# Kernel tuning notes

Hardware: AMD Instinct MI355X
Metric: run time of the kernel (lower is better)

The kernel has to match this reference:

```python
import jax, jax.numpy as jnp
import numpy as np

EPS = 1e-5


def setup_inputs() -> dict:
    key = jax.random.key(0)
    ks = jax.random.split(key, 7)
    N, M, D, H, DM = 8192, 128, 64, 8, 1024  # tokens, num_memories, d_memory, heads, d_model
    return {
        "query": jax.random.normal(ks[0], (N, DM), dtype=jnp.float32),
        "addresses": jax.random.normal(ks[1], (M, D), dtype=jnp.float32),
        "memories": jax.random.normal(ks[2], (N, M, D), dtype=jnp.float32),
        "Wq": jax.random.normal(ks[3], (DM, H * D), dtype=jnp.float32) / np.sqrt(DM),
        "bq": jax.random.normal(ks[4], (H * D,), dtype=jnp.float32) * 0.01,
        "Wo": jax.random.normal(ks[5], (H * D, DM), dtype=jnp.float32) / np.sqrt(H * D),
        "bo": jax.random.normal(ks[6], (DM,), dtype=jnp.float32) * 0.01,
    }


def reference(query, addresses, memories, Wq, bq, Wo, bo):
    N = query.shape[0]
    M, D = addresses.shape
    # Query projection -> heads: (N, H, D)
    q = (query @ Wq + bq).reshape(N, -1, D)
    q = jax.nn.relu(q)  # kernel feature map on query
    # Keys: memory content + learned addresses, kernel feature map
    k = jax.nn.relu(memories + addresses)  # (N, M, D)
    # make_kernel: contract over the num_memories dim
    matrix = jnp.einsum("nmd,nme->nde", k, memories)  # (N, D, D)
    normalizer = jnp.sum(k, axis=-2)  # (N, D)
    # read_from_kernel
    numerator = jnp.einsum("nhd,nde->nhe", q, matrix)  # (N, H, D)
    denominator = jnp.einsum("nhd,nd->nh", q, normalizer)[..., None] + EPS
    attn = numerator / denominator  # (N, H, D)
    # merge heads back to d_model
    return attn.reshape(N, -1) @ Wo + bo
```

## Files before the change

kernel.cpp:

```cpp
#include <hip/hip_runtime.h>

typedef __bf16 bf16x8 __attribute__((ext_vector_type(8)));
typedef __bf16 bf16x4 __attribute__((ext_vector_type(4)));
typedef __bf16 bf16x2 __attribute__((ext_vector_type(2)));
typedef float  f32x4  __attribute__((ext_vector_type(4)));

__global__ __launch_bounds__(256) void transpose_to_bf16(
    const float* __restrict__ src, __bf16* __restrict__ dst, int R, int C)
{
    __shared__ float tile[32][33];
    const int tx = threadIdx.x & 31, ty = threadIdx.x >> 5;
    const int r0 = blockIdx.y * 32, c0 = blockIdx.x * 32;
    #pragma unroll
    for (int i = ty; i < 32; i += 8)
        tile[i][tx] = src[(size_t)(r0 + i) * C + c0 + tx];
    __syncthreads();
    #pragma unroll
    for (int i = ty; i < 32; i += 8)
        dst[(size_t)(c0 + i) * R + r0 + tx] = (__bf16)tile[tx][i];
}

template<int BN, int WM, int WN, bool AF32, bool RELU, bool OBF16>
__global__ __launch_bounds__(256) void gemm_bias(
    const void* __restrict__ Ap, const __bf16* __restrict__ BT,
    const float* __restrict__ bias, void* __restrict__ Outp,
    int M, int N, int K)
{
    constexpr int BM = 128, BK = 32, LD = 40;
    constexpr int FM = BM / WM / 16, FN = BN / WN / 16;
    __shared__ __bf16 As[BM][LD];
    __shared__ __bf16 Bs[BN][LD];

    const int tid  = threadIdx.x;
    const int lane = tid & 63, wid = tid >> 6;
    const int wm = wid / WN, wn = wid % WN;
    const int m0 = blockIdx.y * BM, n0 = blockIdx.x * BN;
    const int r = lane & 15, g = lane >> 4;

    f32x4 acc[FM][FN];
    const f32x4 zero = {0.f, 0.f, 0.f, 0.f};
    #pragma unroll
    for (int mi = 0; mi < FM; ++mi)
        #pragma unroll
        for (int ni = 0; ni < FN; ++ni)
            acc[mi][ni] = zero;

    for (int k0 = 0; k0 < K; k0 += BK) {
        __syncthreads();
        if constexpr (AF32) {
            const float* A = (const float*)Ap;
            #pragma unroll
            for (int i = 0; i < (BM * BK / 4) / 256; ++i) {
                int idx = tid + i * 256;
                int row = idx >> 3, c4 = (idx & 7) * 4;
                f32x4 v = *(const f32x4*)(A + (size_t)(m0 + row) * K + k0 + c4);
                bf16x4 b;
                b[0] = (__bf16)v[0]; b[1] = (__bf16)v[1];
                b[2] = (__bf16)v[2]; b[3] = (__bf16)v[3];
                *(bf16x4*)&As[row][c4] = b;
            }
        } else {
            const __bf16* A = (const __bf16*)Ap;
            #pragma unroll
            for (int i = 0; i < (BM * BK / 8) / 256; ++i) {
                int idx = tid + i * 256;
                int row = idx >> 2, s8 = (idx & 3) * 8;
                *(bf16x8*)&As[row][s8] =
                    *(const bf16x8*)(A + (size_t)(m0 + row) * K + k0 + s8);
            }
        }
        #pragma unroll
        for (int i = 0; i < (BN * 4) / 256; ++i) {
            int idx = tid + i * 256;
            int row = idx >> 2, s8 = (idx & 3) * 8;
            *(bf16x8*)&Bs[row][s8] =
                *(const bf16x8*)(BT + (size_t)(n0 + row) * K + k0 + s8);
        }
        __syncthreads();

        bf16x8 af[FM], bfr[FN];
        #pragma unroll
        for (int mi = 0; mi < FM; ++mi)
            af[mi] = *(const bf16x8*)&As[wm * (FM * 16) + mi * 16 + r][g * 8];
        #pragma unroll
        for (int ni = 0; ni < FN; ++ni)
            bfr[ni] = *(const bf16x8*)&Bs[wn * (FN * 16) + ni * 16 + r][g * 8];
        #pragma unroll
        for (int mi = 0; mi < FM; ++mi)
            #pragma unroll
            for (int ni = 0; ni < FN; ++ni)
                acc[mi][ni] = __builtin_amdgcn_mfma_f32_16x16x32_bf16(
                    af[mi], bfr[ni], acc[mi][ni], 0, 0, 0);
    }

    const int orow = m0 + wm * (FM * 16) + g * 4;
    const int ocol = n0 + wn * (FN * 16) + r;
    #pragma unroll
    for (int ni = 0; ni < FN; ++ni) {
        const float bb = bias[ocol + ni * 16];
        #pragma unroll
        for (int mi = 0; mi < FM; ++mi) {
            #pragma unroll
            for (int q = 0; q < 4; ++q) {
                float v = acc[mi][ni][q] + bb;
                if constexpr (RELU) v = fmaxf(v, 0.f);
                const size_t o = (size_t)(orow + mi * 16 + q) * N + ocol + ni * 16;
                if constexpr (OBF16) ((__bf16*)Outp)[o] = (__bf16)v;
                else                 ((float*)Outp)[o]  = v;
            }
        }
    }
}

__device__ __forceinline__ int kbyte(int m, int e) {
    return m * 128 + ((((e >> 3) ^ (m & 7))) << 4) + (e & 7) * 2;
}

__global__ __launch_bounds__(256) void memory_attn_mfma(
    const __bf16* __restrict__ Q,
    const float*  __restrict__ mem,
    const float*  __restrict__ adr,
    __bf16* __restrict__ attn)
{
    __shared__ __align__(16) unsigned char kbuf[4][4096];
    __shared__ __align__(16) unsigned char tbuf[4][5120];
    __shared__ float denl[4][8];

    const int tid = threadIdx.x, lane = tid & 63, w = tid >> 6;
    const int n = blockIdx.x * 4 + w;
    const int v = lane & 15, g = lane >> 4;

    unsigned char* kb = kbuf[w];
    unsigned char* tb = tbuf[w];

    const __bf16* qp = Q + (size_t)n * 512 + v * 64 + 8 * g;
    const bf16x8 qf0 = *(const bf16x8*)(qp);
    const bf16x8 qf1 = *(const bf16x8*)(qp + 32);

    f32x4 acc[4];
    const f32x4 zero = {0.f, 0.f, 0.f, 0.f};
    #pragma unroll
    for (int nb = 0; nb < 4; ++nb) acc[nb] = zero;
    float psum = 0.f;

    for (int c = 0; c < 4; ++c) {
        const int mb = c * 32;
        #pragma unroll
        for (int i = 0; i < 4; ++i) {
            const int mo = 8 * i + 2 * g;
            const int e  = 4 * v;
            const float* pm = mem + (((size_t)n * 128 + mb + mo) * 64 + e);
            const f32x4 m0 = *(const f32x4*)pm;
            const f32x4 m1 = *(const f32x4*)(pm + 64);
            const float* pav = adr + ((size_t)(mb + mo) * 64 + e);
            const f32x4 a0 = *(const f32x4*)pav;
            const f32x4 a1 = *(const f32x4*)(pav + 64);
            bf16x4 k0, k1;
            #pragma unroll
            for (int j = 0; j < 4; ++j) {
                k0[j] = (__bf16)fmaxf(m0[j] + a0[j], 0.f);
                k1[j] = (__bf16)fmaxf(m1[j] + a1[j], 0.f);
            }
            *(bf16x4*)(kb + kbyte(mo,     e)) = k0;
            *(bf16x4*)(kb + kbyte(mo + 1, e)) = k1;
            const int kap = 8 * ((mo >> 2) & 3) + 4 * (mo >> 4) + (mo & 3);
            #pragma unroll
            for (int j2 = 0; j2 < 4; ++j2) {
                bf16x2 p = { (__bf16)m0[j2], (__bf16)m1[j2] };
                *(bf16x2*)(tb + (size_t)(e + j2) * 80 + kap * 2) = p;
            }
        }

        f32x4 sA0 = zero, sA1 = zero;
        {
            const bf16x8 a00 = *(const bf16x8*)(kb + kbyte(v,      8 * g));
            const bf16x8 a01 = *(const bf16x8*)(kb + kbyte(v,      32 + 8 * g));
            const bf16x8 a10 = *(const bf16x8*)(kb + kbyte(v + 16, 8 * g));
            const bf16x8 a11 = *(const bf16x8*)(kb + kbyte(v + 16, 32 + 8 * g));
            sA0 = __builtin_amdgcn_mfma_f32_16x16x32_bf16(a00, qf0, sA0, 0, 0, 0);
            sA0 = __builtin_amdgcn_mfma_f32_16x16x32_bf16(a01, qf1, sA0, 0, 0, 0);
            sA1 = __builtin_amdgcn_mfma_f32_16x16x32_bf16(a10, qf0, sA1, 0, 0, 0);
            sA1 = __builtin_amdgcn_mfma_f32_16x16x32_bf16(a11, qf1, sA1, 0, 0, 0);
        }
        psum += sA0[0] + sA0[1] + sA0[2] + sA0[3]
              + sA1[0] + sA1[1] + sA1[2] + sA1[3];

        bf16x8 pa;
        #pragma unroll
        for (int q = 0; q < 4; ++q) {
            pa[q]     = (__bf16)sA0[q];
            pa[4 + q] = (__bf16)sA1[q];
        }

        #pragma unroll
        for (int nb = 0; nb < 4; ++nb) {
            const bf16x8 bf = *(const bf16x8*)(tb + (size_t)(16 * nb + v) * 80 + 16 * g);
            acc[nb] = __builtin_amdgcn_mfma_f32_16x16x32_bf16(pa, bf, acc[nb], 0, 0, 0);
        }
    }

    psum += __shfl_xor(psum, 16);
    psum += __shfl_xor(psum, 32);
    if (lane < 8) denl[w][lane] = psum;

    if (g < 2) {
        const f32x4 d4 = *(const f32x4*)&denl[w][4 * g];
        float inv[4];
        #pragma unroll
        for (int q = 0; q < 4; ++q) inv[q] = 1.f / (d4[q] + 1e-5f);
        #pragma unroll
        for (int nb = 0; nb < 4; ++nb) {
            #pragma unroll
            for (int q = 0; q < 4; ++q) {
                attn[(size_t)n * 512 + (4 * g + q) * 64 + 16 * nb + v] =
                    (__bf16)(acc[nb][q] * inv[q]);
            }
        }
    }
}

extern "C" void kernel_launch(void* const* d_in, const int* in_sizes, int n_in,
                              void* d_out, int out_size, void* d_ws, size_t ws_size,
                              hipStream_t stream)
{
    const float* query     = (const float*)d_in[0];
    const float* addresses = (const float*)d_in[1];
    const float* memories  = (const float*)d_in[2];
    const float* Wq        = (const float*)d_in[3];
    const float* bq        = (const float*)d_in[4];
    const float* Wo        = (const float*)d_in[5];
    const float* bo        = (const float*)d_in[6];
    float* out = (float*)d_out;

    char* ws = (char*)d_ws;
    __bf16* WqT = (__bf16*)(ws);
    __bf16* WoT = (__bf16*)(ws + (1 << 20));
    __bf16* Qb  = (__bf16*)(ws + (2 << 20));
    __bf16* Ab  = (__bf16*)(ws + (10 << 20));

    transpose_to_bf16<<<dim3(512 / 32, 1024 / 32), 256, 0, stream>>>(Wq, WqT, 1024, 512);
    transpose_to_bf16<<<dim3(1024 / 32, 512 / 32), 256, 0, stream>>>(Wo, WoT, 512, 1024);

    gemm_bias<64, 4, 1, true, true, true>
        <<<dim3(512 / 64, 8192 / 128), 256, 0, stream>>>(
            query, WqT, bq, Qb, 8192, 512, 1024);

    memory_attn_mfma<<<dim3(8192 / 4), 256, 0, stream>>>(Qb, memories, addresses, Ab);

    gemm_bias<128, 2, 2, false, false, false>
        <<<dim3(1024 / 128, 8192 / 128), 256, 0, stream>>>(
            Ab, WoT, bo, out, 8192, 1024, 512);
}
```

Measured before the change: 128.6 us.

## Use direct global-to-LDS loads in GEMMs, pre-convert inputs, prefetch memories

Replaces the templated GEMM with a fixed 128x128 tile kernel that fills shared memory through global_load_lds 16-byte transfers and drops the padded LDS stride. The query is first converted to bf16 in a separate pass, staged in the output buffer, so the first GEMM reads bf16. The attention kernel now reads pre-converted bf16 addresses and register-prefetches the next chunk of memories while working on the current one, and declares an occupancy hint in its launch bounds. The extra conversion pass adds traffic, and the unpadded LDS layout may cause bank conflicts on fragment reads.

```diff
diff --git a/kernel.cpp b/kernel.cpp
--- a/kernel.cpp
+++ b/kernel.cpp
@@ -5,6 +5,28 @@
 typedef __bf16 bf16x2 __attribute__((ext_vector_type(2)));
 typedef float  f32x4  __attribute__((ext_vector_type(4)));
 
+__device__ __forceinline__ void gload_lds16(const void* g, void* l) {
+    auto gp = reinterpret_cast<const __attribute__((address_space(1))) unsigned int*>(
+        reinterpret_cast<uintptr_t>(g));
+    auto lp = reinterpret_cast<__attribute__((address_space(3))) unsigned int*>(
+        reinterpret_cast<uintptr_t>(l));
+    __builtin_amdgcn_global_load_lds(gp, lp, 16, 0, 0);
+}
+
+__global__ __launch_bounds__(256) void convert_to_bf16(
+    const float* __restrict__ src, __bf16* __restrict__ dst, int n8)
+{
+    const int i = blockIdx.x * 256 + threadIdx.x;
+    if (i < n8) {
+        f32x4 a = ((const f32x4*)src)[2 * i];
+        f32x4 b = ((const f32x4*)src)[2 * i + 1];
+        bf16x8 o;
+        #pragma unroll
+        for (int j = 0; j < 4; ++j) { o[j] = (__bf16)a[j]; o[4 + j] = (__bf16)b[j]; }
+        ((bf16x8*)dst)[i] = o;
+    }
+}
+
 __global__ __launch_bounds__(256) void transpose_to_bf16(
     const float* __restrict__ src, __bf16* __restrict__ dst, int R, int C)
 {
@@ -20,86 +42,62 @@
         dst[(size_t)(c0 + i) * R + r0 + tx] = (__bf16)tile[tx][i];
 }
 
-template<int BN, int WM, int WN, bool AF32, bool RELU, bool OBF16>
-__global__ __launch_bounds__(256) void gemm_bias(
-    const void* __restrict__ Ap, const __bf16* __restrict__ BT,
+template<bool RELU, bool OBF16>
+__global__ __launch_bounds__(256) void gemm_lds(
+    const __bf16* __restrict__ A, const __bf16* __restrict__ BT,
     const float* __restrict__ bias, void* __restrict__ Outp,
     int M, int N, int K)
 {
-    constexpr int BM = 128, BK = 32, LD = 40;
-    constexpr int FM = BM / WM / 16, FN = BN / WN / 16;
-    __shared__ __bf16 As[BM][LD];
-    __shared__ __bf16 Bs[BN][LD];
-
-    const int tid  = threadIdx.x;
-    const int lane = tid & 63, wid = tid >> 6;
-    const int wm = wid / WN, wn = wid % WN;
-    const int m0 = blockIdx.y * BM, n0 = blockIdx.x * BN;
+    __shared__ __bf16 As[128][32];
+    __shared__ __bf16 Bs[128][32];
+
+    const int tid = threadIdx.x, lane = tid & 63, w = tid >> 6;
+    const int wm = w >> 1, wn = w & 1;
+    const int m0 = blockIdx.y * 128, n0 = blockIdx.x * 128;
     const int r = lane & 15, g = lane >> 4;
 
-    f32x4 acc[FM][FN];
+    const int srow = lane >> 2;
+    const int scol = (lane & 3) * 8;
+    const __bf16* gA = A  + (size_t)(m0 + 32 * w + srow) * K + scol;
+    const __bf16* gB = BT + (size_t)(n0 + 32 * w + srow) * K + scol;
+
+    f32x4 acc[4][4];
     const f32x4 zero = {0.f, 0.f, 0.f, 0.f};
     #pragma unroll
-    for (int mi = 0; mi < FM; ++mi)
-        #pragma unroll
-        for (int ni = 0; ni < FN; ++ni)
-            acc[mi][ni] = zero;
-
-    for (int k0 = 0; k0 < K; k0 += BK) {
+    for (int mi = 0; mi < 4; ++mi)
+        #pragma unroll
+        for (int ni = 0; ni < 4; ++ni) acc[mi][ni] = zero;
+
+    for (int k0 = 0; k0 < K; k0 += 32) {
         __syncthreads();
-        if constexpr (AF32) {
-            const float* A = (const float*)Ap;
-            #pragma unroll
-            for (int i = 0; i < (BM * BK / 4) / 256; ++i) {
-                int idx = tid + i * 256;
-                int row = idx >> 3, c4 = (idx & 7) * 4;
-                f32x4 v = *(const f32x4*)(A + (size_t)(m0 + row) * K + k0 + c4);
-                bf16x4 b;
-                b[0] = (__bf16)v[0]; b[1] = (__bf16)v[1];
-                b[2] = (__bf16)v[2]; b[3] = (__bf16)v[3];
-                *(bf16x4*)&As[row][c4] = b;
-            }
-        } else {
-            const __bf16* A = (const __bf16*)Ap;
-            #pragma unroll
-            for (int i = 0; i < (BM * BK / 8) / 256; ++i) {
-                int idx = tid + i * 256;
-                int row = idx >> 2, s8 = (idx & 3) * 8;
-                *(bf16x8*)&As[row][s8] =
-                    *(const bf16x8*)(A + (size_t)(m0 + row) * K + k0 + s8);
-            }
-        }
-        #pragma unroll
-        for (int i = 0; i < (BN * 4) / 256; ++i) {
-            int idx = tid + i * 256;
-            int row = idx >> 2, s8 = (idx & 3) * 8;
-            *(bf16x8*)&Bs[row][s8] =
-                *(const bf16x8*)(BT + (size_t)(n0 + row) * K + k0 + s8);
-        }
+        gload_lds16(gA + k0,          &As[32 * w][0]);
+        gload_lds16(gA + 16 * K + k0, &As[32 * w + 16][0]);
+        gload_lds16(gB + k0,          &Bs[32 * w][0]);
+        gload_lds16(gB + 16 * K + k0, &Bs[32 * w + 16][0]);
         __syncthreads();
 
-        bf16x8 af[FM], bfr[FN];
-        #pragma unroll
-        for (int mi = 0; mi < FM; ++mi)
-            af[mi] = *(const bf16x8*)&As[wm * (FM * 16) + mi * 16 + r][g * 8];
-        #pragma unroll
-        for (int ni = 0; ni < FN; ++ni)
-            bfr[ni] = *(const bf16x8*)&Bs[wn * (FN * 16) + ni * 16 + r][g * 8];
-        #pragma unroll
-        for (int mi = 0; mi < FM; ++mi)
-            #pragma unroll
-            for (int ni = 0; ni < FN; ++ni)
+        bf16x8 af[4], bfr[4];
+        #pragma unroll
+        for (int mi = 0; mi < 4; ++mi)
+            af[mi] = *(const bf16x8*)&As[wm * 64 + mi * 16 + r][g * 8];
+        #pragma unroll
+        for (int ni = 0; ni < 4; ++ni)
+            bfr[ni] = *(const bf16x8*)&Bs[wn * 64 + ni * 16 + r][g * 8];
+        #pragma unroll
+        for (int mi = 0; mi < 4; ++mi)
+            #pragma unroll
+            for (int ni = 0; ni < 4; ++ni)
                 acc[mi][ni] = __builtin_amdgcn_mfma_f32_16x16x32_bf16(
                     af[mi], bfr[ni], acc[mi][ni], 0, 0, 0);
     }
 
-    const int orow = m0 + wm * (FM * 16) + g * 4;
-    const int ocol = n0 + wn * (FN * 16) + r;
-    #pragma unroll
-    for (int ni = 0; ni < FN; ++ni) {
+    const int orow = m0 + wm * 64 + g * 4;
+    const int ocol = n0 + wn * 64 + r;
+    #pragma unroll
+    for (int ni = 0; ni < 4; ++ni) {
         const float bb = bias[ocol + ni * 16];
         #pragma unroll
-        for (int mi = 0; mi < FM; ++mi) {
+        for (int mi = 0; mi < 4; ++mi) {
             #pragma unroll
             for (int q = 0; q < 4; ++q) {
                 float v = acc[mi][ni][q] + bb;
@@ -116,10 +114,10 @@
     return m * 128 + ((((e >> 3) ^ (m & 7))) << 4) + (e & 7) * 2;
 }
 
-__global__ __launch_bounds__(256) void memory_attn_mfma(
+__global__ __launch_bounds__(256, 4) void memory_attn_mfma(
     const __bf16* __restrict__ Q,
     const float*  __restrict__ mem,
-    const float*  __restrict__ adr,
+    const __bf16* __restrict__ adrb,
     __bf16* __restrict__ attn)
 {
     __shared__ __align__(16) unsigned char kbuf[4][4096];
@@ -129,9 +127,11 @@
     const int tid = threadIdx.x, lane = tid & 63, w = tid >> 6;
     const int n = blockIdx.x * 4 + w;
     const int v = lane & 15, g = lane >> 4;
+    const int e4 = 4 * v;
 
     unsigned char* kb = kbuf[w];
     unsigned char* tb = tbuf[w];
+    const float* pmem = mem + (size_t)n * 128 * 64;
 
     const __bf16* qp = Q + (size_t)n * 512 + v * 64 + 8 * g;
     const bf16x8 qf0 = *(const bf16x8*)(qp);
@@ -143,31 +143,46 @@
     for (int nb = 0; nb < 4; ++nb) acc[nb] = zero;
     float psum = 0.f;
 
+    f32x4 cm[8];
+    #pragma unroll
+    for (int i = 0; i < 4; ++i) {
+        const int mo = 8 * i + 2 * g;
+        cm[2 * i]     = *(const f32x4*)(pmem + (size_t)mo * 64 + e4);
+        cm[2 * i + 1] = *(const f32x4*)(pmem + (size_t)(mo + 1) * 64 + e4);
+    }
+
+    #pragma unroll
     for (int c = 0; c < 4; ++c) {
         const int mb = c * 32;
+        f32x4 nm[8];
+        if (c < 3) {
+            #pragma unroll
+            for (int i = 0; i < 4; ++i) {
+                const int mo = mb + 32 + 8 * i + 2 * g;
+                nm[2 * i]     = *(const f32x4*)(pmem + (size_t)mo * 64 + e4);
+                nm[2 * i + 1] = *(const f32x4*)(pmem + (size_t)(mo + 1) * 64 + e4);
+            }
+        }
         #pragma unroll
         for (int i = 0; i < 4; ++i) {
-            const int mo = 8 * i + 2 * g;
-            const int e  = 4 * v;
-            const float* pm = mem + (((size_t)n * 128 + mb + mo) * 64 + e);
-            const f32x4 m0 = *(const f32x4*)pm;
-            const f32x4 m1 = *(const f32x4*)(pm + 64);
-            const float* pav = adr + ((size_t)(mb + mo) * 64 + e);
-            const f32x4 a0 = *(const f32x4*)pav;
-            const f32x4 a1 = *(const f32x4*)(pav + 64);
+            const int mo = mb + 8 * i + 2 * g;
+            const bf16x4 a0 = *(const bf16x4*)(adrb + (size_t)(mo & 127) * 64 + e4);
+            const bf16x4 a1 = *(const bf16x4*)(adrb + (size_t)((mo + 1) & 127) * 64 + e4);
+            const f32x4 m0 = cm[2 * i], m1 = cm[2 * i + 1];
             bf16x4 k0, k1;
             #pragma unroll
             for (int j = 0; j < 4; ++j) {
-                k0[j] = (__bf16)fmaxf(m0[j] + a0[j], 0.f);
-                k1[j] = (__bf16)fmaxf(m1[j] + a1[j], 0.f);
-            }
-            *(bf16x4*)(kb + kbyte(mo,     e)) = k0;
-            *(bf16x4*)(kb + kbyte(mo + 1, e)) = k1;
-            const int kap = 8 * ((mo >> 2) & 3) + 4 * (mo >> 4) + (mo & 3);
+                k0[j] = (__bf16)fmaxf(m0[j] + (float)a0[j], 0.f);
+                k1[j] = (__bf16)fmaxf(m1[j] + (float)a1[j], 0.f);
+            }
+            const int mo_l = mo & 31;
+            *(bf16x4*)(kb + kbyte(mo_l,     e4)) = k0;
+            *(bf16x4*)(kb + kbyte(mo_l + 1, e4)) = k1;
+            const int kap = 8 * ((mo_l >> 2) & 3) + 4 * (mo_l >> 4) + (mo_l & 3);
             #pragma unroll
             for (int j2 = 0; j2 < 4; ++j2) {
                 bf16x2 p = { (__bf16)m0[j2], (__bf16)m1[j2] };
-                *(bf16x2*)(tb + (size_t)(e + j2) * 80 + kap * 2) = p;
+                *(bf16x2*)(tb + (size_t)(e4 + j2) * 80 + kap * 2) = p;
             }
         }
 
@@ -197,6 +212,11 @@
             const bf16x8 bf = *(const bf16x8*)(tb + (size_t)(16 * nb + v) * 80 + 16 * g);
             acc[nb] = __builtin_amdgcn_mfma_f32_16x16x32_bf16(pa, bf, acc[nb], 0, 0, 0);
         }
+
+        if (c < 3) {
+            #pragma unroll
+            for (int t = 0; t < 8; ++t) cm[t] = nm[t];
+        }
     }
 
     psum += __shfl_xor(psum, 16);
@@ -233,21 +253,23 @@
     float* out = (float*)d_out;
 
     char* ws = (char*)d_ws;
-    __bf16* WqT = (__bf16*)(ws);
-    __bf16* WoT = (__bf16*)(ws + (1 << 20));
-    __bf16* Qb  = (__bf16*)(ws + (2 << 20));
-    __bf16* Ab  = (__bf16*)(ws + (10 << 20));
-
+    __bf16* WqT  = (__bf16*)(ws);
+    __bf16* WoT  = (__bf16*)(ws + (1 << 20));
+    __bf16* Qb   = (__bf16*)(ws + (2 << 20));
+    __bf16* Ab   = (__bf16*)(ws + (10 << 20));
+    __bf16* Adrb = (__bf16*)(ws + (18 << 20));
+    __bf16* Qbf  = (__bf16*)d_out;
+
+    convert_to_bf16<<<4096, 256, 0, stream>>>(query, Qbf, 8192 * 1024 / 8);
+    convert_to_bf16<<<4, 256, 0, stream>>>(addresses, Adrb, 128 * 64 / 8);
     transpose_to_bf16<<<dim3(512 / 32, 1024 / 32), 256, 0, stream>>>(Wq, WqT, 1024, 512);
     transpose_to_bf16<<<dim3(1024 / 32, 512 / 32), 256, 0, stream>>>(Wo, WoT, 512, 1024);
 
-    gemm_bias<64, 4, 1, true, true, true>
-        <<<dim3(512 / 64, 8192 / 128), 256, 0, stream>>>(
-            query, WqT, bq, Qb, 8192, 512, 1024);
-
-    memory_attn_mfma<<<dim3(8192 / 4), 256, 0, stream>>>(Qb, memories, addresses, Ab);
-
-    gemm_bias<128, 2, 2, false, false, false>
-        <<<dim3(1024 / 128, 8192 / 128), 256, 0, stream>>>(
-            Ab, WoT, bo, out, 8192, 1024, 512);
-}
+    gemm_lds<true, true><<<dim3(512 / 128, 8192 / 128), 256, 0, stream>>>(
+        Qbf, WqT, bq, Qb, 8192, 512, 1024);
+
+    memory_attn_mfma<<<dim3(8192 / 4), 256, 0, stream>>>(Qb, memories, Adrb, Ab);
+
+    gemm_lds<false, false><<<dim3(1024 / 128, 8192 / 128), 256, 0, stream>>>(
+        Ab, WoT, bo, out, 8192, 1024, 512);
+}
```

Measured after the change: 128.8 us. No clear change (+0.2%).
